# Optimization experiments

Measured on AMD Instinct MI355X. Metric: run time of the kernel, lower is better.

## Reference

```python
import jax, jax.numpy as jnp
import numpy as np

DIM = 512
HEADS = 4
HEAD_DIM = DIM // HEADS
SCALE = HEAD_DIM ** -0.5


def _lin(x, W, b):
    # torch nn.Linear: y = x @ W.T + b, W is [out, in]
    return jnp.einsum('...i,oi->...o', x, W) + b


def setup_inputs() -> dict:
    key = jax.random.key(0)
    ks = jax.random.split(key, 20)
    f1 = jax.random.normal(ks[0], (4, 5, DIM, 10, 10), dtype=jnp.float32)
    f2 = jax.random.normal(ks[1], (4, 75, DIM, 10, 10), dtype=jnp.float32)
    names = ['k1', 'v1', 'q2', 'k2', 'v2', 'o1', 'o2']
    inp = {'f1': f1, 'f2': f2}
    for i, nm in enumerate(names):
        inp['W' + nm] = 0.02 * jax.random.normal(ks[2 + 2 * i], (DIM, DIM), dtype=jnp.float32)
        inp['b' + nm] = 0.02 * jax.random.normal(ks[3 + 2 * i], (DIM,), dtype=jnp.float32)
    return inp


def _forward(f1, f2, Wk1, bk1, Wv1, bv1, Wq2, bq2, Wk2, bk2, Wv2, bv2, Wo1, bo1, Wo2, bo2):
    B, n1, C, H, W = f1.shape
    n2 = f2.shape[1]
    L = H * W
    # [B,n,C,H,W] -> [B,n,L,C]
    f1t = f1.reshape(B, n1, C, L).transpose(0, 1, 3, 2)
    f2t = f2.reshape(B, n2, C, L).transpose(0, 1, 3, 2)

    def split_heads(x, n):  # [B,n,L,C] -> [B,heads,n*L,hd]
        return x.reshape(B, n * L, HEADS, HEAD_DIM).transpose(0, 2, 1, 3)

    def merge_heads(x, n):  # [B,heads,n*L,hd] -> [B,n,L,C]
        return x.transpose(0, 2, 1, 3).reshape(B, n, L, C)

    K1 = split_heads(_lin(f1t, Wk1, bk1), n1)
    V1 = split_heads(_lin(f1t, Wv1, bv1), n1)
    Q2 = split_heads(_lin(f2t, Wq2, bq2), n2)
    K2 = split_heads(_lin(f2t, Wk2, bk2), n2)  # computed as in original, unused downstream
    V2 = split_heads(_lin(f2t, Wv2, bv2), n2)

    # Query attends to support: [B,h,n2*L,n1*L]
    att_q = jax.nn.softmax(jnp.einsum('bhqd,bhkd->bhqk', Q2, K1) * SCALE, axis=-1)
    out2 = jnp.einsum('bhqk,bhkd->bhqd', att_q, V1)
    out2 = _lin(merge_heads(out2, n2), Wo2, bo2)
    out2 = out2.transpose(0, 1, 3, 2).reshape(B, n2, C, H, W)

    # Support attends to query: [B,h,n1*L,n2*L]
    att_s = jax.nn.softmax(jnp.einsum('bhsd,bhqd->bhsq', K1, Q2) * SCALE, axis=-1)
    out1 = jnp.einsum('bhsq,bhqd->bhsd', att_s, V2)
    out1 = _lin(merge_heads(out1, n1), Wo1, bo1)
    out1 = out1.transpose(0, 1, 3, 2).reshape(B, n1, C, H, W)
    return (out1, out2)


def reference(f1, f2, Wk1, bk1, Wv1, bv1, Wq2, bq2, Wk2, bk2, Wv2, bv2, Wo1, bo1, Wo2, bo2):
    return _forward(f1, f2, Wk1, bk1, Wv1, bv1, Wq2, bq2, Wk2, bk2, Wv2, bv2, Wo1, bo1, Wo2, bo2)
```

## Files before the change

kernel.cpp:

```cpp
#include <hip/hip_runtime.h>
#include <hip/hip_bf16.h>


#define QSCL  (0.08838834764831845f * 1.4426950408889634f)
#define KSPL  8
#define NRB2  59
#define NRB1  4

using bf16x8 = __attribute__((ext_vector_type(8))) short;
using f32x4  = __attribute__((ext_vector_type(4))) float;

__device__ inline ushort f2bf(float x) {
    union { float f; unsigned u; } v; v.f = x;
    unsigned r = v.u + 0x7fff + ((v.u >> 16) & 1);
    return (ushort)(r >> 16);
}

__device__ inline void gll16(const ushort* g, ushort* l) {
    __builtin_amdgcn_global_load_lds(
        (const __attribute__((address_space(1))) void*)g,
        (__attribute__((address_space(3))) void*)l, 16, 0, 0);
}

struct PreArgs { const float* w[6]; float s[6]; const float* f1; const float* f2; };

__global__ __launch_bounds__(256) void pre_kernel(
    PreArgs pa, ushort* __restrict__ Wb,
    ushort* __restrict__ f1t, ushort* __restrict__ f2t)
{
    __shared__ ushort Ts[100 * 136];
    const int t   = threadIdx.x;
    const int bid = blockIdx.x;

    if (bid < 1536) {
        const int wsel = bid >> 8;
        const float* src = pa.w[wsel];
        const float sc = pa.s[wsel];
        ushort* d = Wb + (size_t)wsel * 262144;
        const int idx = ((bid & 255) * 256 + t) * 4;
        const float4 v = *(const float4*)(src + idx);
        ushort4 o;
        o.x = f2bf(v.x * sc); o.y = f2bf(v.y * sc);
        o.z = f2bf(v.z * sc); o.w = f2bf(v.w * sc);
        *(ushort4*)(d + idx) = o;
        return;
    }

    const int bn = bid - 1536;
    const float* Xb;
    ushort* Yb;
    if (bn < 20) { Xb = pa.f1 + (size_t)bn * 51200;        Yb = f1t + (size_t)bn * 51200; }
    else         { Xb = pa.f2 + (size_t)(bn - 20) * 51200; Yb = f2t + (size_t)(bn - 20) * 51200; }

    for (int c0 = 0; c0 < 512; c0 += 128) {
        __syncthreads();
        #pragma unroll
        for (int i = 0; i < 50; ++i) {
            const int id = i * 256 + t;
            const int c = id / 100, l = id - c * 100;
            Ts[l * 136 + c] = f2bf(Xb[(size_t)(c0 + c) * 100 + l]);
        }
        __syncthreads();
        #pragma unroll
        for (int i = 0; i < 7; ++i) {
            const int id = i * 256 + t;
            if (id < 1600) {
                const int cg = id & 15, l = id >> 4;
                *(uint4*)(Yb + (size_t)l * 512 + c0 + cg * 8) =
                    *(const uint4*)&Ts[l * 136 + cg * 8];
            }
        }
    }
}

struct GemmJob {
    const ushort* A; const ushort* B;
    const float* bias; void* C;
    size_t sA, sB, sC;
    float bscale;
    int ldC, Mrows, Ncols, gx, gy, fastn, baxis, nblk;
};

struct GemmJobs { GemmJob j0, j1, j2, j3; int ntot; };

template<int EPI>
__global__ __launch_bounds__(256) void gemm_nt(GemmJobs J)
{
    __shared__ ushort smem[17408];
    ushort* As = smem;
    ushort* Bs = smem + 8192;

    const int ntot = J.ntot;
    const int q8 = ntot >> 3, r8 = ntot & 7;
    const int xcd = blockIdx.x & 7, ii = blockIdx.x >> 3;
    const int work = (xcd < r8 ? xcd * (q8 + 1)
                               : r8 * (q8 + 1) + (xcd - r8) * q8) + ii;

    GemmJob j; int id;
    {
        const int c0 = J.j0.nblk;
        const int c1 = c0 + J.j1.nblk;
        const int c2 = c1 + J.j2.nblk;
        if (work < c0)      { j = J.j0; id = work; }
        else if (work < c1) { j = J.j1; id = work - c0; }
        else if (work < c2) { j = J.j2; id = work - c1; }
        else                { j = J.j3; id = work - c2; }
    }

    const int fx = id % j.gx;
    const int rem = id / j.gx;
    const int fy = rem % j.gy;
    const int bz = rem / j.gy;
    const int m0 = (j.fastn ? fy : fx) * 128;
    const int n0 = (j.fastn ? fx : fy) * 128;

    const int t    = threadIdx.x;
    const int lane = t & 63;
    const int w    = t >> 6;
    const int mw   = (w >> 1) * 64;
    const int nw   = (w & 1) * 64;
    const int Mrows = j.Mrows, Ncols = j.Ncols, ldC = j.ldC;
    const ushort* Ab = j.A + (size_t)bz * j.sA;
    const ushort* Bb = j.B + (size_t)bz * j.sB;
    const float* bias = j.bias;

    f32x4 acc[4][4];
    #pragma unroll
    for (int i = 0; i < 4; ++i)
        #pragma unroll
        for (int jj = 0; jj < 4; ++jj) acc[i][jj] = (f32x4){0.f, 0.f, 0.f, 0.f};

    const int lr = lane >> 3;
    const int cb = lane & 7;

    for (int k0 = 0; k0 < 512; k0 += 64) {
        if (k0) __syncthreads();
        #pragma unroll
        for (int i = 0; i < 4; ++i) {
            const int row = w * 32 + i * 8 + lr;
            const int ar = min(m0 + row, Mrows - 1);
            gll16(Ab + (size_t)ar * 512 + k0 + ((cb ^ (row & 7)) * 8),
                  As + (w * 32 + i * 8) * 64);
            const int br = min(n0 + row, Ncols - 1);
            gll16(Bb + (size_t)br * 512 + k0 + ((cb ^ (row & 7)) * 8),
                  Bs + (w * 32 + i * 8) * 64);
        }
        __syncthreads();
        #pragma unroll
        for (int ks = 0; ks < 2; ++ks) {
            bf16x8 af[4], bv[4];
            #pragma unroll
            for (int mf = 0; mf < 4; ++mf) {
                const int row = mw + mf * 16 + (lane & 15);
                af[mf] = *(const bf16x8*)((const char*)As + row * 128 +
                          ((ks * 64 + (lane >> 4) * 16) ^ ((row & 7) << 4)));
            }
            #pragma unroll
            for (int nf = 0; nf < 4; ++nf) {
                const int row = nw + nf * 16 + (lane & 15);
                bv[nf] = *(const bf16x8*)((const char*)Bs + row * 128 +
                          ((ks * 64 + (lane >> 4) * 16) ^ ((row & 7) << 4)));
            }
            #pragma unroll
            for (int mf = 0; mf < 4; ++mf)
                #pragma unroll
                for (int nf = 0; nf < 4; ++nf)
                    acc[mf][nf] = __builtin_amdgcn_mfma_f32_16x16x32_bf16(
                        af[mf], bv[nf], acc[mf][nf], 0, 0, 0);
        }
    }
    __syncthreads();

    if (EPI == 0) {
        float bcol[4];
        if (j.baxis == 1) {
            #pragma unroll
            for (int nf = 0; nf < 4; ++nf)
                bcol[nf] = bias[n0 + nw + nf * 16 + (lane & 15)] * j.bscale;
        }
        ushort* Ts = smem;
        #pragma unroll
        for (int mf = 0; mf < 4; ++mf) {
            #pragma unroll
            for (int r = 0; r < 4; ++r) {
                const int row = mw + mf * 16 + (lane >> 4) * 4 + r;
                const float brow = (j.baxis == 0) ? bias[m0 + row] * j.bscale : 0.f;
                #pragma unroll
                for (int nf = 0; nf < 4; ++nf) {
                    const int col = nw + nf * 16 + (lane & 15);
                    const float v = acc[mf][nf][r] +
                                    ((j.baxis == 1) ? bcol[nf] : brow);
                    Ts[row * 136 + col] = f2bf(v);
                }
            }
        }
        __syncthreads();
        ushort* Cb = (ushort*)j.C + (size_t)bz * j.sC;
        #pragma unroll
        for (int i = 0; i < 8; ++i) {
            const int id2 = i * 256 + t;
            const int row = id2 >> 4, cg = id2 & 15;
            if (m0 + row < Mrows)
                *(uint4*)(Cb + (size_t)(m0 + row) * ldC + n0 + cg * 8) =
                    *(const uint4*)&Ts[row * 136 + cg * 8];
        }
    } else {
        float* Ts2 = (float*)smem;
        float* Cb = (float*)j.C + (size_t)bz * j.sC;
        const int colL = t & 127;
        const int rb2 = t >> 7;
        const int tg = n0 + colL;
        int nIdx = 0, lIdx = 0;
        if (tg < Ncols) { nIdx = tg / 100; lIdx = tg - nIdx * 100; }
        #pragma unroll
        for (int h = 0; h < 2; ++h) {
            __syncthreads();
            if ((mw >> 6) == h) {
                #pragma unroll
                for (int mf = 0; mf < 4; ++mf) {
                    #pragma unroll
                    for (int r = 0; r < 4; ++r) {
                        const int rowl = mf * 16 + (lane >> 4) * 4 + r;
                        const float brow = bias[m0 + h * 64 + rowl];
                        #pragma unroll
                        for (int nf = 0; nf < 4; ++nf) {
                            const int col = nw + nf * 16 + (lane & 15);
                            Ts2[rowl * 132 + col] = acc[mf][nf][r] + brow;
                        }
                    }
                }
            }
            __syncthreads();
            if (tg < Ncols) {
                float* dst = Cb + (size_t)nIdx * 51200 + lIdx;
                #pragma unroll
                for (int i = 0; i < 32; ++i) {
                    const int rowl = i * 2 + rb2;
                    const int c = m0 + h * 64 + rowl;
                    dst[(size_t)c * 100] = Ts2[rowl * 132 + colL];
                }
            }
        }
    }
}

__global__ __launch_bounds__(512, 4) void attn_mfma_kernel(
    const ushort* __restrict__ Q2, const ushort* __restrict__ K1,
    const ushort* __restrict__ V1t, const ushort* __restrict__ V2t,
    ushort* __restrict__ A2, float* __restrict__ PartO, float* __restrict__ Pml)
{
    __shared__ ushort Ks[64 * 128];
    __shared__ ushort Vs[128 * 64];

    const int t    = threadIdx.x;
    const int lane = t & 63;
    const int w    = t >> 6;

    const int flat = blockIdx.x;
    const int xcd = flat & 7, ii = flat >> 3;
    const bool dir2 = (ii >= 64);
    int rb, h, b, sp = 0;
    if (dir2) {
        const int w2 = xcd * 118 + (ii - 64);
        rb = w2 % NRB2;
        const int hb = w2 / NRB2;
        h = hb & 3; b = hb >> 2;
    } else {
        const int w1 = xcd * 64 + ii;
        rb = w1 & 3; sp = (w1 >> 2) & 7;
        const int hb = w1 >> 5;
        h = hb & 3; b = hb >> 2;
    }

    const int TR = dir2 ? 7500 : 500;
    const int TK = dir2 ? 500 : 7500;
    const int strideV = dir2 ? 512 : 7552;
    const ushort* R  = dir2 ? Q2 : K1;
    const ushort* Kt = dir2 ? K1 : Q2;
    const ushort* Vt = dir2 ? V1t : V2t;

    const int r0 = rb * 128;
    const int ho = h * 128;

    int kbeg = 0, kend = TK;
    if (!dir2) {
        kbeg = sp * 938;
        kend = kbeg + 938; if (kend > TK) kend = TK;
    }

    bf16x8 qa[4];
    {
        const ushort* Rb = R + (size_t)b * TR * 512;
        const int qrow = min(r0 + (w << 4) + (lane & 15), TR - 1);
        const ushort* qp = Rb + (size_t)qrow * 512 + ho + (lane >> 4) * 8;
        #pragma unroll
        for (int s = 0; s < 4; ++s)
            qa[s] = *(const bf16x8*)(qp + s * 32);
    }

    const ushort* Kb = Kt + (size_t)b * TK * 512;
    const ushort* Vb = Vt + ((size_t)b * 512 + ho) * strideV;

    const int krow_i = lane >> 4;
    const int kcol   = (lane & 15) * 8;
    const int vrow_i = lane >> 3;
    const int vcol   = (lane & 7) * 8;
    const int gq     = lane >> 4;

    float m_run = -3.0e38f, l_run = 0.f;
    f32x4 acc[8];
    #pragma unroll
    for (int g = 0; g < 8; ++g) acc[g] = (f32x4){0.f, 0.f, 0.f, 0.f};

    #pragma unroll
    for (int i = 0; i < 2; ++i) {
        const int kr = w * 8 + i * 4 + krow_i;
        gll16(Kb + (size_t)(kbeg + kr) * 512 + ho + (kcol ^ ((kr & 7) << 3)),
              Ks + (w * 8 + i * 4) * 128);
    }

    for (int kbase = kbeg; kbase < kend; kbase += 64) {
        #pragma unroll
        for (int i = 0; i < 2; ++i) {
            const int vd = w * 16 + i * 8 + vrow_i;
            gll16(Vb + (size_t)vd * strideV + kbase + (vcol ^ ((vd & 7) << 3)),
                  Vs + (w * 16 + i * 8) * 64);
        }
        asm volatile("s_waitcnt vmcnt(2)" ::: "memory");
        __builtin_amdgcn_s_barrier();
        __builtin_amdgcn_sched_barrier(0);

        f32x4 sf[4];
        __builtin_amdgcn_s_setprio(1);
        #pragma unroll
        for (int f = 0; f < 4; ++f) {
            f32x4 s = (f32x4){0.f, 0.f, 0.f, 0.f};
            const int kr = f * 16 + (lane & 15);
            const int kb2 = kr * 256, sw = (kr & 7) << 4, g16 = gq * 16;
            #pragma unroll
            for (int s4 = 0; s4 < 4; ++s4) {
                bf16x8 kf = *(const bf16x8*)((const char*)Ks + kb2 + ((s4 * 64 + g16) ^ sw));
                s = __builtin_amdgcn_mfma_f32_16x16x32_bf16(kf, qa[s4], s, 0, 0, 0);
            }
            sf[f] = s;
        }
        __builtin_amdgcn_s_setprio(0);

        if (kbase + 64 > kend) {
            #pragma unroll
            for (int f = 0; f < 4; ++f)
                #pragma unroll
                for (int r = 0; r < 4; ++r)
                    if (kbase + f * 16 + gq * 4 + r >= kend) sf[f][r] = -3.0e38f;
        }
        float mx = sf[0][0];
        #pragma unroll
        for (int f = 0; f < 4; ++f)
            #pragma unroll
            for (int r = 0; r < 4; ++r) mx = fmaxf(mx, sf[f][r]);
        mx = fmaxf(mx, __shfl_xor(mx, 16));
        mx = fmaxf(mx, __shfl_xor(mx, 32));
        if (__any(mx > m_run + 11.0f)) {
            const float mn = fmaxf(m_run, mx);
            const float sc = __builtin_amdgcn_exp2f(m_run - mn);
            m_run = mn;
            l_run *= sc;
            float scal4[4];
            #pragma unroll
            for (int r = 0; r < 4; ++r)
                scal4[r] = __shfl(sc, (lane & 48) + gq * 4 + r);
            #pragma unroll
            for (int g = 0; g < 8; ++g)
                #pragma unroll
                for (int r = 0; r < 4; ++r) acc[g][r] *= scal4[r];
        }
        float rs = 0.f;
        #pragma unroll
        for (int f = 0; f < 4; ++f)
            #pragma unroll
            for (int r = 0; r < 4; ++r) {
                const float p = __builtin_amdgcn_exp2f(sf[f][r] - m_run);
                sf[f][r] = p;
                rs += p;
            }
        rs += __shfl_xor(rs, 16);
        rs += __shfl_xor(rs, 32);
        l_run += rs;

        uint pk[4][2];
        #pragma unroll
        for (int f = 0; f < 4; ++f) {
            const float x0 = sf[f][0], x1 = sf[f][1], x2 = sf[f][2], x3 = sf[f][3];
            asm("v_cvt_pk_bf16_f32 %0, %1, %2" : "=v"(pk[f][0]) : "v"(x0), "v"(x1));
            asm("v_cvt_pk_bf16_f32 %0, %1, %2" : "=v"(pk[f][1]) : "v"(x2), "v"(x3));
        }
        union { uint u[4]; bf16x8 v; } pa0, pa1;
        #pragma unroll
        for (int u = 0; u < 4; ++u) {
            const int srcl = (lane & 15) + ((lane & 16) << 1) + ((u >> 1) << 4);
            const uint a0 = (uint)__shfl((int)pk[0][u & 1], srcl);
            const uint b0 = (uint)__shfl((int)pk[1][u & 1], srcl);
            const uint a1 = (uint)__shfl((int)pk[2][u & 1], srcl);
            const uint b1 = (uint)__shfl((int)pk[3][u & 1], srcl);
            pa0.u[u] = (lane & 32) ? b0 : a0;
            pa1.u[u] = (lane & 32) ? b1 : a1;
        }

        asm volatile("s_waitcnt vmcnt(0)" ::: "memory");
        __builtin_amdgcn_s_barrier();
        __builtin_amdgcn_sched_barrier(0);

        if (kbase + 64 < kend) {
            #pragma unroll
            for (int i = 0; i < 2; ++i) {
                const int kr = w * 8 + i * 4 + krow_i;
                gll16(Kb + (size_t)(kbase + 64 + kr) * 512 + ho + (kcol ^ ((kr & 7) << 3)),
                      Ks + (w * 8 + i * 4) * 128);
            }
        }

        {
            const int g16 = gq * 16;
            __builtin_amdgcn_s_setprio(1);
            #pragma unroll
            for (int g = 0; g < 8; ++g) {
                const int dr = g * 16 + (lane & 15);
                const int vb = dr * 128, vsw = (dr & 7) << 4;
                bf16x8 v0 = *(const bf16x8*)((const char*)Vs + vb + ((g16) ^ vsw));
                bf16x8 v1 = *(const bf16x8*)((const char*)Vs + vb + ((64 + g16) ^ vsw));
                acc[g] = __builtin_amdgcn_mfma_f32_16x16x32_bf16(pa0.v, v0, acc[g], 0, 0, 0);
                acc[g] = __builtin_amdgcn_mfma_f32_16x16x32_bf16(pa1.v, v1, acc[g], 0, 0, 0);
            }
            __builtin_amdgcn_s_setprio(0);
        }
        __builtin_amdgcn_s_barrier();
        __builtin_amdgcn_sched_barrier(0);
    }

    const int rloc = (w << 4) + (gq << 2);
    if (dir2) {
        float linv[4];
        #pragma unroll
        for (int r = 0; r < 4; ++r)
            linv[r] = 1.f / __shfl(l_run, (lane & 48) + gq * 4 + r);
        #pragma unroll
        for (int r = 0; r < 4; ++r) {
            const int row = r0 + rloc + r;
            if (row < TR) {
                ushort* Ab2 = A2 + ((size_t)b * TR + row) * 512 + ho + (lane & 15);
                #pragma unroll
                for (int g = 0; g < 8; ++g) Ab2[g * 16] = f2bf(acc[g][r] * linv[r]);
            }
        }
    } else {
        const size_t tile = (((size_t)b * 4 + h) * NRB1 + rb) * KSPL + sp;
        float* Po = PartO + tile * (128 * 128);
        float* Pm = Pml + tile * 256;
        #pragma unroll
        for (int r = 0; r < 4; ++r) {
            const int row = rloc + r;
            float* pp = Po + row * 128 + (lane & 15);
            #pragma unroll
            for (int g = 0; g < 8; ++g) pp[g * 16] = acc[g][r];
        }
        if (lane < 16) {
            Pm[(w << 4) + lane] = m_run;
            Pm[128 + (w << 4) + lane] = l_run;
        }
    }
}

__global__ __launch_bounds__(256) void attn_combine_kernel(
    const float* __restrict__ PartO, const float* __restrict__ Pml,
    ushort* __restrict__ Aout, int TR)
{
    const int t = threadIdx.x;
    const int rb = blockIdx.x >> 1, half = blockIdx.x & 1;
    const int h = blockIdx.y, b = blockIdx.z;
    const int row = half * 64 + (t >> 2);
    const int dq = (t & 3) * 32;
    const int r0 = rb * 128;
    const size_t tbase = (((size_t)b * 4 + h) * NRB1 + rb) * KSPL;

    float M = -3.0e38f;
    #pragma unroll
    for (int i = 0; i < KSPL; ++i)
        M = fmaxf(M, Pml[(tbase + i) * 256 + row]);
    float wt[KSPL], L = 0.f;
    #pragma unroll
    for (int i = 0; i < KSPL; ++i) {
        const float wi = __builtin_amdgcn_exp2f(Pml[(tbase + i) * 256 + row] - M);
        wt[i] = wi;
        L += wi * Pml[(tbase + i) * 256 + 128 + row];
    }
    if (r0 + row >= TR) return;
    const float invL = 1.f / L;

    float o[32];
    #pragma unroll
    for (int j = 0; j < 32; ++j) o[j] = 0.f;
    #pragma unroll
    for (int i = 0; i < KSPL; ++i) {
        const float* pp = PartO + (tbase + i) * (128 * 128) + row * 128 + dq;
        #pragma unroll
        for (int j = 0; j < 32; j += 4) {
            const float4 v = *(const float4*)(pp + j);
            o[j] += wt[i] * v.x; o[j+1] += wt[i] * v.y;
            o[j+2] += wt[i] * v.z; o[j+3] += wt[i] * v.w;
        }
    }
    ushort* Ab = Aout + ((size_t)b * TR + r0 + row) * 512 + h * 128 + dq;
    #pragma unroll
    for (int j = 0; j < 32; j += 4) {
        ushort4 v;
        v.x = f2bf(o[j] * invL); v.y = f2bf(o[j+1] * invL);
        v.z = f2bf(o[j+2] * invL); v.w = f2bf(o[j+3] * invL);
        *(ushort4*)(Ab + j) = v;
    }
}

extern "C" void kernel_launch(void* const* d_in, const int* in_sizes, int n_in,
                              void* d_out, int out_size, void* d_ws, size_t ws_size,
                              hipStream_t stream) {
    const float* f1  = (const float*)d_in[0];
    const float* f2  = (const float*)d_in[1];
    const float* Wk1 = (const float*)d_in[2];
    const float* bk1 = (const float*)d_in[3];
    const float* Wv1 = (const float*)d_in[4];
    const float* bv1 = (const float*)d_in[5];
    const float* Wq2 = (const float*)d_in[6];
    const float* bq2 = (const float*)d_in[7];
    const float* Wv2 = (const float*)d_in[10];
    const float* bv2 = (const float*)d_in[11];
    const float* Wo1 = (const float*)d_in[12];
    const float* bo1 = (const float*)d_in[13];
    const float* Wo2 = (const float*)d_in[14];
    const float* bo2 = (const float*)d_in[15];
    float* out = (float*)d_out;

    ushort* f1t = (ushort*)d_ws;
    ushort* f2t = f1t + (size_t)1024000;
    ushort* Wb  = f2t + (size_t)15360000;
    ushort* K1  = Wb  + (size_t)1572864;
    ushort* Q2  = K1  + (size_t)1024000;
    ushort* V1t = Q2  + (size_t)15360000;
    ushort* V2t = V1t + (size_t)1048576;
    ushort* A1  = V2t + (size_t)15466496;
    ushort* A2  = A1  + (size_t)1024000;
    float* PartO = (float*)(A2 + (size_t)15360000);
    float* Pml   = PartO + (size_t)512*128*128;

    const dim3 blk(256);

    const ushort* Wk1b = Wb;
    const ushort* Wv1b = Wb + 262144;
    const ushort* Wq2b = Wb + 2*262144;
    const ushort* Wv2b = Wb + 3*262144;
    const ushort* Wo1b = Wb + 4*262144;
    const ushort* Wo2b = Wb + 5*262144;

    PreArgs pa;
    pa.w[0]=Wk1; pa.w[1]=Wv1; pa.w[2]=Wq2; pa.w[3]=Wv2; pa.w[4]=Wo1; pa.w[5]=Wo2;
    pa.s[0]=1.f; pa.s[1]=1.f; pa.s[2]=QSCL; pa.s[3]=1.f; pa.s[4]=1.f; pa.s[5]=1.f;
    pa.f1 = f1; pa.f2 = f2;
    pre_kernel<<<dim3(1856), blk, 0, stream>>>(pa, Wb, f1t, f2t);

    GemmJob jK {f1t, Wk1b, bk1, K1, 0, 0, 0, 1.f, 512, 2000, 512,
                4, 16, 1, 1, 64};
    GemmJob jQ {f2t, Wq2b, bq2, Q2, 0, 0, 0, QSCL, 512, 30000, 512,
                4, 235, 1, 1, 940};
    GemmJob jV1{Wv1b, f1t, bv1, V1t, 0, (size_t)500*512, (size_t)512*512, 1.f,
                512, 512, 500, 4, 4, 0, 0, 64};
    GemmJob jV2{Wv2b, f2t, bv2, V2t, 0, (size_t)7500*512, (size_t)512*7552, 1.f,
                7552, 512, 7500, 4, 59, 0, 0, 944};
    GemmJobs JP{jK, jQ, jV1, jV2, 2012};
    gemm_nt<0><<<dim3(2012), blk, 0, stream>>>(JP);

    attn_mfma_kernel<<<dim3(1456), dim3(512), 0, stream>>>(
        Q2, K1, V1t, V2t, A2, PartO, Pml);
    attn_combine_kernel<<<dim3(8, 4, 4), blk, 0, stream>>>(PartO, Pml, A1, 500);

    GemmJob jO1{Wo1b, A1, bo1, out, 0, (size_t)500*512, (size_t)5*51200, 1.f,
                0, 512, 500, 4, 4, 0, 0, 64};
    GemmJob jO2{Wo2b, A2, bo2, out + (size_t)1024000, 0, (size_t)7500*512,
                (size_t)75*51200, 1.f, 0, 512, 7500, 4, 59, 0, 0, 944};
    GemmJob jZ{};
    GemmJobs JO{jO1, jO2, jZ, jZ, 1008};
    gemm_nt<2><<<dim3(1008), blk, 0, stream>>>(JO);
}
```

Baseline: 238.1 us.

## Process two 16-row query tiles per wave in attention kernel with 4 waves

```diff
diff --git a/kernel.cpp b/kernel.cpp
--- a/kernel.cpp
+++ b/kernel.cpp
@@ -244,7 +244,7 @@
     }
 }
 
-__global__ __launch_bounds__(512, 4) void attn_mfma_kernel(
+__global__ __launch_bounds__(256, 3) void attn_mfma_kernel(
     const ushort* __restrict__ Q2, const ushort* __restrict__ K1,
     const ushort* __restrict__ V1t, const ushort* __restrict__ V2t,
     ushort* __restrict__ A2, float* __restrict__ PartO, float* __restrict__ Pml)
@@ -288,14 +288,18 @@
         kend = kbeg + 938; if (kend > TK) kend = TK;
     }
 
-    bf16x8 qa[4];
+    bf16x8 qa0[4], qa1[4];
     {
         const ushort* Rb = R + (size_t)b * TR * 512;
-        const int qrow = min(r0 + (w << 4) + (lane & 15), TR - 1);
-        const ushort* qp = Rb + (size_t)qrow * 512 + ho + (lane >> 4) * 8;
-        #pragma unroll
-        for (int s = 0; s < 4; ++s)
-            qa[s] = *(const bf16x8*)(qp + s * 32);
+        const int q0 = min(r0 + w * 32 + (lane & 15), TR - 1);
+        const int q1 = min(r0 + w * 32 + 16 + (lane & 15), TR - 1);
+        const ushort* qp0 = Rb + (size_t)q0 * 512 + ho + (lane >> 4) * 8;
+        const ushort* qp1 = Rb + (size_t)q1 * 512 + ho + (lane >> 4) * 8;
+        #pragma unroll
+        for (int s = 0; s < 4; ++s) {
+            qa0[s] = *(const bf16x8*)(qp0 + s * 32);
+            qa1[s] = *(const bf16x8*)(qp1 + s * 32);
+        }
     }
 
     const ushort* Kb = Kt + (size_t)b * TK * 512;
@@ -307,42 +311,48 @@
     const int vcol   = (lane & 7) * 8;
     const int gq     = lane >> 4;
 
-    float m_run = -3.0e38f, l_run = 0.f;
-    f32x4 acc[8];
-    #pragma unroll
-    for (int g = 0; g < 8; ++g) acc[g] = (f32x4){0.f, 0.f, 0.f, 0.f};
-
-    #pragma unroll
-    for (int i = 0; i < 2; ++i) {
-        const int kr = w * 8 + i * 4 + krow_i;
+    float m_run0 = -3.0e38f, l_run0 = 0.f;
+    float m_run1 = -3.0e38f, l_run1 = 0.f;
+    f32x4 acc0[8], acc1[8];
+    #pragma unroll
+    for (int g = 0; g < 8; ++g) {
+        acc0[g] = (f32x4){0.f, 0.f, 0.f, 0.f};
+        acc1[g] = (f32x4){0.f, 0.f, 0.f, 0.f};
+    }
+
+    #pragma unroll
+    for (int i = 0; i < 4; ++i) {
+        const int kr = w * 16 + i * 4 + krow_i;
         gll16(Kb + (size_t)(kbeg + kr) * 512 + ho + (kcol ^ ((kr & 7) << 3)),
-              Ks + (w * 8 + i * 4) * 128);
+              Ks + (w * 16 + i * 4) * 128);
     }
 
     for (int kbase = kbeg; kbase < kend; kbase += 64) {
         #pragma unroll
-        for (int i = 0; i < 2; ++i) {
-            const int vd = w * 16 + i * 8 + vrow_i;
+        for (int i = 0; i < 4; ++i) {
+            const int vd = w * 32 + i * 8 + vrow_i;
             gll16(Vb + (size_t)vd * strideV + kbase + (vcol ^ ((vd & 7) << 3)),
-                  Vs + (w * 16 + i * 8) * 64);
-        }
-        asm volatile("s_waitcnt vmcnt(2)" ::: "memory");
+                  Vs + (w * 32 + i * 8) * 64);
+        }
+        asm volatile("s_waitcnt vmcnt(4)" ::: "memory");
         __builtin_amdgcn_s_barrier();
         __builtin_amdgcn_sched_barrier(0);
 
-        f32x4 sf[4];
+        f32x4 sf0[4], sf1[4];
         __builtin_amdgcn_s_setprio(1);
         #pragma unroll
         for (int f = 0; f < 4; ++f) {
-            f32x4 s = (f32x4){0.f, 0.f, 0.f, 0.f};
+            f32x4 s0 = (f32x4){0.f, 0.f, 0.f, 0.f};
+            f32x4 s1 = (f32x4){0.f, 0.f, 0.f, 0.f};
             const int kr = f * 16 + (lane & 15);
             const int kb2 = kr * 256, sw = (kr & 7) << 4, g16 = gq * 16;
             #pragma unroll
             for (int s4 = 0; s4 < 4; ++s4) {
                 bf16x8 kf = *(const bf16x8*)((const char*)Ks + kb2 + ((s4 * 64 + g16) ^ sw));
-                s = __builtin_amdgcn_mfma_f32_16x16x32_bf16(kf, qa[s4], s, 0, 0, 0);
-            }
-            sf[f] = s;
+                s0 = __builtin_amdgcn_mfma_f32_16x16x32_bf16(kf, qa0[s4], s0, 0, 0, 0);
+                s1 = __builtin_amdgcn_mfma_f32_16x16x32_bf16(kf, qa1[s4], s1, 0, 0, 0);
+            }
+            sf0[f] = s0; sf1[f] = s1;
         }
         __builtin_amdgcn_s_setprio(0);
 
@@ -351,59 +361,103 @@
             for (int f = 0; f < 4; ++f)
                 #pragma unroll
                 for (int r = 0; r < 4; ++r)
-                    if (kbase + f * 16 + gq * 4 + r >= kend) sf[f][r] = -3.0e38f;
-        }
-        float mx = sf[0][0];
-        #pragma unroll
-        for (int f = 0; f < 4; ++f)
-            #pragma unroll
-            for (int r = 0; r < 4; ++r) mx = fmaxf(mx, sf[f][r]);
-        mx = fmaxf(mx, __shfl_xor(mx, 16));
-        mx = fmaxf(mx, __shfl_xor(mx, 32));
-        if (__any(mx > m_run + 11.0f)) {
-            const float mn = fmaxf(m_run, mx);
-            const float sc = __builtin_amdgcn_exp2f(m_run - mn);
-            m_run = mn;
-            l_run *= sc;
-            float scal4[4];
-            #pragma unroll
-            for (int r = 0; r < 4; ++r)
-                scal4[r] = __shfl(sc, (lane & 48) + gq * 4 + r);
-            #pragma unroll
-            for (int g = 0; g < 8; ++g)
-                #pragma unroll
-                for (int r = 0; r < 4; ++r) acc[g][r] *= scal4[r];
-        }
-        float rs = 0.f;
-        #pragma unroll
-        for (int f = 0; f < 4; ++f)
-            #pragma unroll
-            for (int r = 0; r < 4; ++r) {
-                const float p = __builtin_amdgcn_exp2f(sf[f][r] - m_run);
-                sf[f][r] = p;
-                rs += p;
-            }
-        rs += __shfl_xor(rs, 16);
-        rs += __shfl_xor(rs, 32);
-        l_run += rs;
-
-        uint pk[4][2];
-        #pragma unroll
-        for (int f = 0; f < 4; ++f) {
-            const float x0 = sf[f][0], x1 = sf[f][1], x2 = sf[f][2], x3 = sf[f][3];
-            asm("v_cvt_pk_bf16_f32 %0, %1, %2" : "=v"(pk[f][0]) : "v"(x0), "v"(x1));
-            asm("v_cvt_pk_bf16_f32 %0, %1, %2" : "=v"(pk[f][1]) : "v"(x2), "v"(x3));
-        }
-        union { uint u[4]; bf16x8 v; } pa0, pa1;
-        #pragma unroll
-        for (int u = 0; u < 4; ++u) {
-            const int srcl = (lane & 15) + ((lane & 16) << 1) + ((u >> 1) << 4);
-            const uint a0 = (uint)__shfl((int)pk[0][u & 1], srcl);
-            const uint b0 = (uint)__shfl((int)pk[1][u & 1], srcl);
-            const uint a1 = (uint)__shfl((int)pk[2][u & 1], srcl);
-            const uint b1 = (uint)__shfl((int)pk[3][u & 1], srcl);
-            pa0.u[u] = (lane & 32) ? b0 : a0;
-            pa1.u[u] = (lane & 32) ? b1 : a1;
+                    if (kbase + f * 16 + gq * 4 + r >= kend) {
+                        sf0[f][r] = -3.0e38f; sf1[f][r] = -3.0e38f;
+                    }
+        }
+        {
+            float mx = sf0[0][0];
+            #pragma unroll
+            for (int f = 0; f < 4; ++f)
+                #pragma unroll
+                for (int r = 0; r < 4; ++r) mx = fmaxf(mx, sf0[f][r]);
+            mx = fmaxf(mx, __shfl_xor(mx, 16));
+            mx = fmaxf(mx, __shfl_xor(mx, 32));
+            if (__any(mx > m_run0 + 11.0f)) {
+                const float mn = fmaxf(m_run0, mx);
+                const float sc = __builtin_amdgcn_exp2f(m_run0 - mn);
+                m_run0 = mn; l_run0 *= sc;
+                float scal4[4];
+                #pragma unroll
+                for (int r = 0; r < 4; ++r)
+                    scal4[r] = __shfl(sc, (lane & 48) + gq * 4 + r);
+                #pragma unroll
+                for (int g = 0; g < 8; ++g)
+                    #pragma unroll
+                    for (int r = 0; r < 4; ++r) acc0[g][r] *= scal4[r];
+            }
+            float rs = 0.f;
+            #pragma unroll
+            for (int f = 0; f < 4; ++f)
+                #pragma unroll
+                for (int r = 0; r < 4; ++r) {
+                    const float p = __builtin_amdgcn_exp2f(sf0[f][r] - m_run0);
+                    sf0[f][r] = p; rs += p;
+                }
+            rs += __shfl_xor(rs, 16);
+            rs += __shfl_xor(rs, 32);
+            l_run0 += rs;
+        }
+        {
+            float mx = sf1[0][0];
+            #pragma unroll
+            for (int f = 0; f < 4; ++f)
+                #pragma unroll
+                for (int r = 0; r < 4; ++r) mx = fmaxf(mx, sf1[f][r]);
+            mx = fmaxf(mx, __shfl_xor(mx, 16));
+            mx = fmaxf(mx, __shfl_xor(mx, 32));
+            if (__any(mx > m_run1 + 11.0f)) {
+                const float mn = fmaxf(m_run1, mx);
+                const float sc = __builtin_amdgcn_exp2f(m_run1 - mn);
+                m_run1 = mn; l_run1 *= sc;
+                float scal4[4];
+                #pragma unroll
+                for (int r = 0; r < 4; ++r)
+                    scal4[r] = __shfl(sc, (lane & 48) + gq * 4 + r);
+                #pragma unroll
+                for (int g = 0; g < 8; ++g)
+                    #pragma unroll
+                    for (int r = 0; r < 4; ++r) acc1[g][r] *= scal4[r];
+            }
+            float rs = 0.f;
+            #pragma unroll
+            for (int f = 0; f < 4; ++f)
+                #pragma unroll
+                for (int r = 0; r < 4; ++r) {
+                    const float p = __builtin_amdgcn_exp2f(sf1[f][r] - m_run1);
+                    sf1[f][r] = p; rs += p;
+                }
+            rs += __shfl_xor(rs, 16);
+            rs += __shfl_xor(rs, 32);
+            l_run1 += rs;
+        }
+
+        union { uint u[4]; bf16x8 v; } pa00, pa01, pa10, pa11;
+        {
+            uint pk0[4][2], pk1[4][2];
+            #pragma unroll
+            for (int f = 0; f < 4; ++f) {
+                asm("v_cvt_pk_bf16_f32 %0, %1, %2" : "=v"(pk0[f][0]) : "v"(sf0[f][0]), "v"(sf0[f][1]));
+                asm("v_cvt_pk_bf16_f32 %0, %1, %2" : "=v"(pk0[f][1]) : "v"(sf0[f][2]), "v"(sf0[f][3]));
+                asm("v_cvt_pk_bf16_f32 %0, %1, %2" : "=v"(pk1[f][0]) : "v"(sf1[f][0]), "v"(sf1[f][1]));
+                asm("v_cvt_pk_bf16_f32 %0, %1, %2" : "=v"(pk1[f][1]) : "v"(sf1[f][2]), "v"(sf1[f][3]));
+            }
+            #pragma unroll
+            for (int u = 0; u < 4; ++u) {
+                const int srcl = (lane & 15) + ((lane & 16) << 1) + ((u >> 1) << 4);
+                const uint a0 = (uint)__shfl((int)pk0[0][u & 1], srcl);
+                const uint b0 = (uint)__shfl((int)pk0[1][u & 1], srcl);
+                const uint a1 = (uint)__shfl((int)pk0[2][u & 1], srcl);
+                const uint b1 = (uint)__shfl((int)pk0[3][u & 1], srcl);
+                pa00.u[u] = (lane & 32) ? b0 : a0;
+                pa01.u[u] = (lane & 32) ? b1 : a1;
+                const uint c0 = (uint)__shfl((int)pk1[0][u & 1], srcl);
+                const uint d0 = (uint)__shfl((int)pk1[1][u & 1], srcl);
+                const uint c1 = (uint)__shfl((int)pk1[2][u & 1], srcl);
+                const uint d1 = (uint)__shfl((int)pk1[3][u & 1], srcl);
+                pa10.u[u] = (lane & 32) ? d0 : c0;
+                pa11.u[u] = (lane & 32) ? d1 : c1;
+            }
         }
 
         asm volatile("s_waitcnt vmcnt(0)" ::: "memory");
@@ -412,10 +466,10 @@
 
         if (kbase + 64 < kend) {
             #pragma unroll
-            for (int i = 0; i < 2; ++i) {
-                const int kr = w * 8 + i * 4 + krow_i;
+            for (int i = 0; i < 4; ++i) {
+                const int kr = w * 16 + i * 4 + krow_i;
                 gll16(Kb + (size_t)(kbase + 64 + kr) * 512 + ho + (kcol ^ ((kr & 7) << 3)),
-                      Ks + (w * 8 + i * 4) * 128);
+                      Ks + (w * 16 + i * 4) * 128);
             }
         }
 
@@ -428,8 +482,10 @@
                 const int vb = dr * 128, vsw = (dr & 7) << 4;
                 bf16x8 v0 = *(const bf16x8*)((const char*)Vs + vb + ((g16) ^ vsw));
                 bf16x8 v1 = *(const bf16x8*)((const char*)Vs + vb + ((64 + g16) ^ vsw));
-                acc[g] = __builtin_amdgcn_mfma_f32_16x16x32_bf16(pa0.v, v0, acc[g], 0, 0, 0);
-                acc[g] = __builtin_amdgcn_mfma_f32_16x16x32_bf16(pa1.v, v1, acc[g], 0, 0, 0);
+                acc0[g] = __builtin_amdgcn_mfma_f32_16x16x32_bf16(pa00.v, v0, acc0[g], 0, 0, 0);
+                acc0[g] = __builtin_amdgcn_mfma_f32_16x16x32_bf16(pa01.v, v1, acc0[g], 0, 0, 0);
+                acc1[g] = __builtin_amdgcn_mfma_f32_16x16x32_bf16(pa10.v, v0, acc1[g], 0, 0, 0);
+                acc1[g] = __builtin_amdgcn_mfma_f32_16x16x32_bf16(pa11.v, v1, acc1[g], 0, 0, 0);
             }
             __builtin_amdgcn_s_setprio(0);
         }
@@ -437,19 +493,26 @@
         __builtin_amdgcn_sched_barrier(0);
     }
 
-    const int rloc = (w << 4) + (gq << 2);
     if (dir2) {
-        float linv[4];
-        #pragma unroll
-        for (int r = 0; r < 4; ++r)
-            linv[r] = 1.f / __shfl(l_run, (lane & 48) + gq * 4 + r);
+        float linv0[4], linv1[4];
         #pragma unroll
         for (int r = 0; r < 4; ++r) {
-            const int row = r0 + rloc + r;
-            if (row < TR) {
-                ushort* Ab2 = A2 + ((size_t)b * TR + row) * 512 + ho + (lane & 15);
-                #pragma unroll
-                for (int g = 0; g < 8; ++g) Ab2[g * 16] = f2bf(acc[g][r] * linv[r]);
+            linv0[r] = 1.f / __shfl(l_run0, (lane & 48) + gq * 4 + r);
+            linv1[r] = 1.f / __shfl(l_run1, (lane & 48) + gq * 4 + r);
+        }
+        #pragma unroll
+        for (int r = 0; r < 4; ++r) {
+            const int row0 = r0 + w * 32 + (gq << 2) + r;
+            if (row0 < TR) {
+                ushort* Ab2 = A2 + ((size_t)b * TR + row0) * 512 + ho + (lane & 15);
+                #pragma unroll
+                for (int g = 0; g < 8; ++g) Ab2[g * 16] = f2bf(acc0[g][r] * linv0[r]);
+            }
+            const int row1 = r0 + w * 32 + 16 + (gq << 2) + r;
+            if (row1 < TR) {
+                ushort* Ab2 = A2 + ((size_t)b * TR + row1) * 512 + ho + (lane & 15);
+                #pragma unroll
+                for (int g = 0; g < 8; ++g) Ab2[g * 16] = f2bf(acc1[g][r] * linv1[r]);
             }
         }
     } else {
@@ -458,14 +521,20 @@
         float* Pm = Pml + tile * 256;
         #pragma unroll
         for (int r = 0; r < 4; ++r) {
-            const int row = rloc + r;
-            float* pp = Po + row * 128 + (lane & 15);
-            #pragma unroll
-            for (int g = 0; g < 8; ++g) pp[g * 16] = acc[g][r];
+            const int row0 = w * 32 + (gq << 2) + r;
+            float* pp0 = Po + row0 * 128 + (lane & 15);
+            #pragma unroll
+            for (int g = 0; g < 8; ++g) pp0[g * 16] = acc0[g][r];
+            const int row1 = w * 32 + 16 + (gq << 2) + r;
+            float* pp1 = Po + row1 * 128 + (lane & 15);
+            #pragma unroll
+            for (int g = 0; g < 8; ++g) pp1[g * 16] = acc1[g][r];
         }
         if (lane < 16) {
-            Pm[(w << 4) + lane] = m_run;
-            Pm[128 + (w << 4) + lane] = l_run;
+            Pm[w * 32 + lane] = m_run0;
+            Pm[w * 32 + 16 + lane] = m_run1;
+            Pm[128 + w * 32 + lane] = l_run0;
+            Pm[128 + w * 32 + 16 + lane] = l_run1;
         }
     }
 }
@@ -576,7 +645,7 @@
     GemmJobs JP{jK, jQ, jV1, jV2, 2012};
     gemm_nt<0><<<dim3(2012), blk, 0, stream>>>(JP);
 
-    attn_mfma_kernel<<<dim3(1456), dim3(512), 0, stream>>>(
+    attn_mfma_kernel<<<dim3(1456), dim3(256), 0, stream>>>(
         Q2, K1, V1t, V2t, A2, PartO, Pml);
     attn_combine_kernel<<<dim3(8, 4, 4), blk, 0, stream>>>(PartO, Pml, A1, 500);
 
```

Result: slower. 308.4 us (+29.5%).
